# Kernel tuning notes

Measured on AMD Instinct MI355X. Metric: run time of the kernel, lower is better.

Reference implementation:

```python
import jax, jax.numpy as jnp
import numpy as np

SEQ_LEN = 2048
N_FFT = 4096   # rfft length n >= seq_len (repo uses next power of two of ~2*seq)
K = 24         # num_eigh
D = 768        # n_embd
BATCH = 1


def _spectral_filters(seq_len: int, k: int) -> jnp.ndarray:
    # Hankel matrix Z[i,j] = 2 / ((i+j)^3 - (i+j)), 1-indexed
    e = np.arange(1, seq_len + 1, dtype=np.float64)
    ipj = e[:, None] + e[None, :]
    Z = 2.0 / (ipj ** 3 - ipj)
    sigma, phi = np.linalg.eigh(Z)
    sigma, phi = sigma[-k:], phi[:, -k:]
    phi = phi * sigma ** 0.25
    return jnp.asarray(phi, dtype=jnp.float32)  # (seq_len, K)


def setup_inputs() -> dict:
    key = jax.random.key(0)
    k1, k2, k3 = jax.random.split(key, 3)
    x = jax.random.normal(k1, (BATCH, SEQ_LEN, D), dtype=jnp.float32)
    M_phi_plus = jax.random.normal(k2, (K, D, D), dtype=jnp.float32) * 0.02
    M_phi_minus = jax.random.normal(k3, (K, D, D), dtype=jnp.float32) * 0.02
    phi = _spectral_filters(SEQ_LEN, K)
    return {"x": x, "phi": phi, "M_phi_plus": M_phi_plus, "M_phi_minus": M_phi_minus}


def _convolve(u, v, n):
    # u: (b, seq, d), v: (seq, K)
    bsz, seq, d = u.shape
    k = v.shape[1]
    # alternating sign sequence (+1, -1, +1, ...)
    sgn = jnp.where(jnp.arange(seq) % 2 == 1, -1.0, 1.0)[None, :, None, None]  # (1,seq,1,1)
    V = jnp.fft.rfft(v.reshape(1, seq, k, 1, 1).astype(jnp.float32), n=n, axis=1)
    u4 = jnp.broadcast_to(u[:, :, None, :], (bsz, seq, k, d))  # (b,seq,K,d)
    U = jnp.stack([u4, u4 * sgn], axis=-1).astype(jnp.float32)  # (b,seq,K,d,2)
    Uf = jnp.fft.rfft(U, n=n, axis=1)
    U_conv = jnp.fft.irfft(V * Uf, n=n, axis=1)[:, :seq]  # (b,seq,K,d,2)
    U_plus = U_conv[..., 0]
    U_minus = U_conv[..., 1] * sgn
    return U_plus, U_minus


def reference(x, phi, M_phi_plus, M_phi_minus):
    U_plus, U_minus = _convolve(x, phi, N_FFT)
    spectral_plus = jnp.einsum('bskd,kde->bse', U_plus, M_phi_plus)
    spectral_minus = jnp.einsum('bskd,kde->bse', U_minus, M_phi_minus)
    return spectral_plus + spectral_minus
```

## Files before the change

### kernel.cpp

```cpp
#include <hip/hip_runtime.h>
#include <hip/hip_bf16.h>
#include <stdint.h>

#define SEQ 2048
#define DDIM 768
#define KF 24
#define NKV 48
#define NZC 8

typedef unsigned short ushort_t;
typedef __attribute__((ext_vector_type(8))) short short8;
typedef __attribute__((ext_vector_type(4))) float f32x4;

typedef __attribute__((address_space(3))) uint32_t lds_u32;
typedef __attribute__((address_space(1))) uint32_t glb_u32;

__device__ __forceinline__ unsigned short f2bf(float f) {
    union { float f; uint32_t u; } v; v.f = f;
    uint32_t u = v.u;
    return (unsigned short)((u + 0x7fff + ((u >> 16) & 1)) >> 16);
}


__global__ void k_pack_x(const float* __restrict__ x, ushort_t* __restrict__ xpk) {
    int b = blockIdx.x;
    int tt = b / 12, ks = b % 12;
    int tid = threadIdx.x;
    ushort_t* dst = xpk + (size_t)b * 8192;
    const float* src = x + (size_t)tt * 128 * DDIM + ks * 64;
#pragma unroll
    for (int p = 0; p < 4; ++p) {
        int s = p * 256 + tid;
        int row = s >> 3, sl = s & 7;
        const float* rp = src + (size_t)row * DDIM + sl * 8;
        float4 a = *(const float4*)rp;
        float4 c = *(const float4*)(rp + 4);
        ushort_t v[8] = {f2bf(a.x), f2bf(a.y), f2bf(a.z), f2bf(a.w),
                         f2bf(c.x), f2bf(c.y), f2bf(c.z), f2bf(c.w)};
        *(uint4*)(dst + row * 64 + ((sl ^ (row & 7)) << 3)) = *(uint4*)v;
    }
}

__global__ void k_pack_M(const float* __restrict__ Mp, const float* __restrict__ Mm,
                         ushort_t* __restrict__ Mpk) {
    __shared__ ushort_t lt[128 * 66];
    int b = blockIdx.x;
    int kv = b / 72; int rem = b % 72; int et = rem / 12, ks = rem % 12;
    const float* src = ((kv < KF) ? Mp + (size_t)kv * DDIM * DDIM
                                  : Mm + (size_t)(kv - KF) * DDIM * DDIM)
                       + (size_t)(ks * 64) * DDIM + et * 128;
    int tid = threadIdx.x;
#pragma unroll
    for (int p = 0; p < 32; ++p) {
        int lin = p * 256 + tid;
        int d = lin >> 7, e = lin & 127;
        lt[e * 66 + d] = f2bf(src[(size_t)d * DDIM + e]);
    }
    __syncthreads();
    ushort_t* dst = Mpk + (size_t)b * 8192;
#pragma unroll
    for (int p = 0; p < 4; ++p) {
        int s = p * 256 + tid; int row = s >> 3, sl = s & 7;
        ushort_t v[8];
#pragma unroll
        for (int j = 0; j < 8; ++j) v[j] = lt[row * 66 + sl * 8 + j];
        *(uint4*)(dst + row * 64 + ((sl ^ (row & 7)) << 3)) = *(uint4*)v;
    }
}

__global__ void k_build_T(const float* __restrict__ phi, ushort_t* __restrict__ Tpk) {
    __shared__ float phiL[256];
    int b = blockIdx.x;
    int kv = b / 17, slot = b % 17;
    int dm = slot - 1;
    int k = kv % KF; bool neg = kv >= KF;
    int tid = threadIdx.x;
    int tau = 128 * dm - 127 + tid;
    float v = 0.f;
    if (tid < 255 && tau >= 0 && tau < SEQ) {
        v = phi[(size_t)tau * KF + k];
        if (neg && (tau & 1)) v = -v;
    }
    phiL[tid] = v;
    __syncthreads();
    ushort_t* dst = Tpk + (size_t)b * 2 * 8192;
#pragma unroll
    for (int h = 0; h < 2; ++h) {
#pragma unroll
        for (int p = 0; p < 4; ++p) {
            int s = p * 256 + tid; int row = s >> 3, sl = s & 7;
            ushort_t v8[8];
#pragma unroll
            for (int j = 0; j < 8; ++j) {
                int col = h * 64 + sl * 8 + j;
                v8[j] = f2bf(phiL[row - col + 127]);
            }
            *(uint4*)(dst + h * 8192 + row * 64 + ((sl ^ (row & 7)) << 3)) = *(uint4*)v8;
        }
    }
}


__device__ __forceinline__ void read_frags(const ushort_t* As, const ushort_t* Bs,
                                           int lane, int wm, int wn, int kk,
                                           short8 av[4], short8 bv[4]) {
    int slot = kk * 4 + (lane >> 4);
#pragma unroll
    for (int m = 0; m < 4; ++m) {
        int row = wm * 64 + m * 16 + (lane & 15);
        av[m] = *(const short8*)(As + row * 64 + ((slot ^ (row & 7)) << 3));
    }
#pragma unroll
    for (int n = 0; n < 4; ++n) {
        int row = wn * 64 + n * 16 + (lane & 15);
        bv[n] = *(const short8*)(Bs + row * 64 + ((slot ^ (row & 7)) << 3));
    }
}

__device__ __forceinline__ void mfma16(const short8 av[4], const short8 bv[4], f32x4 acc[4][4]) {
    __builtin_amdgcn_s_setprio(1);
#pragma unroll
    for (int m = 0; m < 4; ++m)
#pragma unroll
        for (int n = 0; n < 4; ++n)
            acc[m][n] = __builtin_amdgcn_mfma_f32_16x16x32_bf16(av[m], bv[n], acc[m][n], 0, 0, 0);
    __builtin_amdgcn_s_setprio(0);
}

__global__ __launch_bounds__(256, 2)
void k_gemm_A(const ushort_t* __restrict__ Mpk, const ushort_t* __restrict__ xpk,
              ushort_t* __restrict__ Apk) {
    __shared__ ushort_t smem[2][2][8192];
    int bid = blockIdx.x;
    int kv = bid / 96; int rem = bid % 96; int et = rem / 16, tt = rem % 16;
    const ushort_t* Abase = Mpk + ((size_t)(kv * 6 + et) * 12) * 8192;
    const ushort_t* Bbase = xpk + (size_t)(tt * 12) * 8192;
    int tid = threadIdx.x, lane = tid & 63, wave = tid >> 6;
    int wm = wave >> 1, wn = wave & 1;

    auto stage4 = [&](const ushort_t* src, ushort_t* dst) {
        const char* s = (const char*)src + wave * 4096 + lane * 16;
        char* l = (char*)dst + wave * 4096;
#pragma unroll
        for (int p = 0; p < 4; ++p)
            __builtin_amdgcn_global_load_lds((const glb_u32*)(s + p * 1024),
                                             (lds_u32*)(l + p * 1024), 16, 0, 0);
    };

    f32x4 acc[4][4];
#pragma unroll
    for (int m = 0; m < 4; ++m)
#pragma unroll
        for (int n = 0; n < 4; ++n) acc[m][n] = (f32x4){0.f, 0.f, 0.f, 0.f};

    stage4(Abase, smem[0][0]);
    stage4(Bbase, smem[0][1]);

    for (int s = 0; s < 12; ++s) {
        int c = s & 1;
        bool more = (s + 1 < 12);
        if (more) {
            stage4(Abase + (s + 1) * 8192, smem[c ^ 1][0]);
            asm volatile("s_waitcnt vmcnt(4)" ::: "memory");
        } else {
            asm volatile("s_waitcnt vmcnt(0)" ::: "memory");
        }
        __builtin_amdgcn_s_barrier();
        __builtin_amdgcn_sched_barrier(0);

        const ushort_t* As = smem[c][0];
        const ushort_t* Bs = smem[c][1];
        short8 av0[4], bv0[4], av1[4], bv1[4];
        read_frags(As, Bs, lane, wm, wn, 0, av0, bv0);
        asm volatile("s_waitcnt lgkmcnt(0)" ::: "memory");
        __builtin_amdgcn_sched_barrier(0);
        read_frags(As, Bs, lane, wm, wn, 1, av1, bv1);
        if (more) stage4(Bbase + (s + 1) * 8192, smem[c ^ 1][1]);
        mfma16(av0, bv0, acc);
        asm volatile("s_waitcnt lgkmcnt(0)" ::: "memory");
        __builtin_amdgcn_sched_barrier(0);
        mfma16(av1, bv1, acc);
        __builtin_amdgcn_s_barrier();
    }

    ushort_t* sm = &smem[0][0][0];
#pragma unroll
    for (int m = 0; m < 4; ++m) {
        int rb = wm * 64 + m * 16 + ((lane >> 4) << 2);
#pragma unroll
        for (int n = 0; n < 4; ++n) {
            int cb = wn * 64 + n * 16 + (lane & 15);
            int h = cb >> 6, c6 = cb & 63, sl = c6 >> 3, j = c6 & 7;
#pragma unroll
            for (int r = 0; r < 4; ++r) {
                int row = rb + r;
                sm[h * 8192 + row * 64 + ((sl ^ (row & 7)) << 3) + j] = f2bf(acc[m][n][r]);
            }
        }
    }
    __syncthreads();
    uint4* d4 = (uint4*)(Apk + ((size_t)((kv * 6 + et) * 16 + tt) * 2) * 8192);
    const uint4* s4 = (const uint4*)sm;
#pragma unroll
    for (int p = 0; p < 8; ++p) d4[p * 256 + tid] = s4[p * 256 + tid];
}

__global__ __launch_bounds__(256, 2)
void k_gemm_Bv4(const ushort_t* __restrict__ Tpk, const ushort_t* __restrict__ Apk,
                float* __restrict__ outz) {
    __shared__ ushort_t smem[2][2][8192];

    int bid = blockIdx.x;
    int lid = (bid & 7) * 54 + (bid >> 3);
    int et = lid / 72;
    int cidx = lid % 72;
    int i1 = 0, zc = 0, base = 0;
#pragma unroll
    for (int t = 0; t < 16; ++t) {
        int cand = 15 - t;
        int nc = (cand >> 1) + 1;
        if (cidx < base + nc) { i1 = cand; zc = cidx - base; break; }
        base += nc;
    }
    int jlo = zc * 2;
    const int NS = NKV * 2 * 2;

    int tid = threadIdx.x, lane = tid & 63, wave = tid >> 6;
    int wm = wave >> 1, wn = wave & 1;

    f32x4 acc[4][4];
#pragma unroll
    for (int m = 0; m < 4; ++m)
#pragma unroll
        for (int n = 0; n < 4; ++n) acc[m][n] = (f32x4){0.f, 0.f, 0.f, 0.f};

    auto timg = [&](int kv, int jj, int h) -> const ushort_t* {
        return Tpk + ((size_t)((kv * 17 + (i1 - jj + 1)) * 2 + h)) * 8192;
    };
    auto aimg = [&](int kv, int jj, int h) -> const ushort_t* {
        return Apk + ((size_t)(((kv * 6 + et) * 16 + jj) * 2 + h)) * 8192;
    };
    auto stage4 = [&](const ushort_t* src, ushort_t* dst) {
        const char* s = (const char*)src + wave * 4096 + lane * 16;
        char* l = (char*)dst + wave * 4096;
#pragma unroll
        for (int p = 0; p < 4; ++p)
            __builtin_amdgcn_global_load_lds((const glb_u32*)(s + p * 1024),
                                             (lds_u32*)(l + p * 1024), 16, 0, 0);
    };

    int kv = 0, jj = jlo, h = 0;
    stage4(timg(kv, jj, h), smem[0][0]);
    stage4(aimg(kv, jj, h), smem[0][1]);

    for (int s = 0; s < NS; ++s) {
        int c = s & 1;
        int nh = h ^ 1, njj = jj, nkvv = kv;
        if (!nh) { njj = jj + 1; if (njj > jlo + 1) { njj = jlo; nkvv = kv + 1; } }
        bool more = (s + 1 < NS);

        if (more) {
            stage4(timg(nkvv, njj, nh), smem[c ^ 1][0]);
            asm volatile("s_waitcnt vmcnt(4)" ::: "memory");
        } else {
            asm volatile("s_waitcnt vmcnt(0)" ::: "memory");
        }
        __builtin_amdgcn_s_barrier();
        __builtin_amdgcn_sched_barrier(0);

        const ushort_t* As = smem[c][0];
        const ushort_t* Bs = smem[c][1];
        short8 av[2][4], bv[2][4];
#pragma unroll
        for (int kk = 0; kk < 2; ++kk) {
            int slot = kk * 4 + (lane >> 4);
#pragma unroll
            for (int m = 0; m < 4; ++m) {
                int row = wm * 64 + m * 16 + (lane & 15);
                av[kk][m] = *(const short8*)(As + row * 64 + ((slot ^ (row & 7)) << 3));
            }
#pragma unroll
            for (int n = 0; n < 4; ++n) {
                int row = wn * 64 + n * 16 + (lane & 15);
                bv[kk][n] = *(const short8*)(Bs + row * 64 + ((slot ^ (row & 7)) << 3));
            }
        }
        if (more) stage4(aimg(nkvv, njj, nh), smem[c ^ 1][1]);

        asm volatile("s_waitcnt lgkmcnt(0)" ::: "memory");
        __builtin_amdgcn_sched_barrier(0);

        __builtin_amdgcn_s_setprio(1);
#pragma unroll
        for (int kk = 0; kk < 2; ++kk)
#pragma unroll
            for (int m = 0; m < 4; ++m)
#pragma unroll
                for (int n = 0; n < 4; ++n)
                    acc[m][n] = __builtin_amdgcn_mfma_f32_16x16x32_bf16(av[kk][m], bv[kk][n], acc[m][n], 0, 0, 0);
        __builtin_amdgcn_s_setprio(0);
        __builtin_amdgcn_s_barrier();
        kv = nkvv; jj = njj; h = nh;
    }

    float* dst = outz + ((size_t)zc * SEQ + (size_t)i1 * 128) * DDIM + et * 128;
#pragma unroll
    for (int m = 0; m < 4; ++m) {
        int rb = wm * 64 + m * 16 + ((lane >> 4) << 2);
#pragma unroll
        for (int n = 0; n < 4; ++n) {
            int cb = wn * 64 + n * 16 + (lane & 15);
#pragma unroll
            for (int r = 0; r < 4; ++r)
                dst[(size_t)(rb + r) * DDIM + cb] = acc[m][n][r];
        }
    }
}

__global__ void k_reduce(const float* __restrict__ outz, float* __restrict__ out, int n4) {
    int idx = blockIdx.x * blockDim.x + threadIdx.x;
    if (idx < n4) {
        int srow = idx / (DDIM / 4);
        int zmax = srow >> 8;
        if (zmax > NZC - 1) zmax = NZC - 1;
        float4 s = ((const float4*)outz)[idx];
        for (int z = 1; z <= zmax; ++z) {
            float4 t = ((const float4*)(outz + (size_t)z * SEQ * DDIM))[idx];
            s.x += t.x; s.y += t.y; s.z += t.z; s.w += t.w;
        }
        ((float4*)out)[idx] = s;
    }
}

extern "C" void kernel_launch(void* const* d_in, const int* in_sizes, int n_in,
                              void* d_out, int out_size, void* d_ws, size_t ws_size,
                              hipStream_t stream) {
    (void)in_sizes; (void)n_in;
    const float* x   = (const float*)d_in[0];
    const float* phi = (const float*)d_in[1];
    const float* Mp  = (const float*)d_in[2];
    const float* Mm  = (const float*)d_in[3];
    float* out = (float*)d_out;

    char* ws = (char*)d_ws;
    size_t off = 0;
    auto alloc = [&](size_t bytes) { size_t o = off; off += (bytes + 255) & ~(size_t)255; return o; };
    size_t o_xpk = alloc((size_t)16 * 12 * 8192 * 2);
    size_t o_Mpk = alloc((size_t)NKV * 6 * 12 * 8192 * 2);
    size_t o_Tpk = alloc((size_t)NKV * 17 * 2 * 8192 * 2);
    size_t o_Apk = alloc((size_t)NKV * 6 * 16 * 2 * 8192 * 2);
    if (off > ws_size) {
        hipMemsetAsync(d_out, 0, (size_t)out_size * 4, stream);
        return;
    }

    ushort_t* xpk = (ushort_t*)(ws + o_xpk);
    ushort_t* Mpk = (ushort_t*)(ws + o_Mpk);
    ushort_t* Tpk = (ushort_t*)(ws + o_Tpk);
    ushort_t* Apk = (ushort_t*)(ws + o_Apk);
    float*   outz = (float*)(ws + o_Mpk);

    k_pack_x<<<16 * 12, 256, 0, stream>>>(x, xpk);
    k_pack_M<<<NKV * 6 * 12, 256, 0, stream>>>(Mp, Mm, Mpk);
    k_build_T<<<NKV * 17, 256, 0, stream>>>(phi, Tpk);
    k_gemm_A<<<NKV * 96, 256, 0, stream>>>(Mpk, xpk, Apk);
    k_gemm_Bv4<<<432, 256, 0, stream>>>(Tpk, Apk, outz);
    int n4 = SEQ * DDIM / 4;
    k_reduce<<<(n4 + 255) / 256, 256, 0, stream>>>(outz, out, n4);
}
```

Before: 328.2 us.

## Stream-K schedule for Toeplitz GEMM with per-tile partial slabs and reduce

Replaces the uneven triangular tile split (432 blocks, each doing a fixed 192 k-steps on chunk pairs) with a stream-K decomposition. The full linearized iteration space of 78336 steps is divided evenly over 512 blocks of 153 steps each. Each block flushes a partial 128x128 tile to a slab whenever its output tile changes, and the reduce kernel sums the partial slabs covering each tile. The goal is better load balance and fuller use of the CUs, at the cost of extra partial-tile stores and a different reduce pattern.

```diff
diff --git a/kernel.cpp b/kernel.cpp
--- a/kernel.cpp
+++ b/kernel.cpp
@@ -6,7 +6,6 @@
 #define DDIM 768
 #define KF 24
 #define NKV 48
-#define NZC 8
 
 typedef unsigned short ushort_t;
 typedef __attribute__((ext_vector_type(8))) short short8;
@@ -206,24 +205,33 @@
 }
 
 __global__ __launch_bounds__(256, 2)
-void k_gemm_Bv4(const ushort_t* __restrict__ Tpk, const ushort_t* __restrict__ Apk,
-                float* __restrict__ outz) {
+void k_gemm_Bsk(const ushort_t* __restrict__ Tpk, const ushort_t* __restrict__ Apk,
+                float* __restrict__ slab) {
     __shared__ ushort_t smem[2][2][8192];
 
     int bid = blockIdx.x;
-    int lid = (bid & 7) * 54 + (bid >> 3);
-    int et = lid / 72;
-    int cidx = lid % 72;
-    int i1 = 0, zc = 0, base = 0;
-#pragma unroll
-    for (int t = 0; t < 16; ++t) {
-        int cand = 15 - t;
-        int nc = (cand >> 1) + 1;
-        if (cidx < base + nc) { i1 = cand; zc = cidx - base; break; }
-        base += nc;
-    }
-    int jlo = zc * 2;
-    const int NS = NKV * 2 * 2;
+    int lid = (bid & 7) * 64 + (bid >> 3);
+    int g0 = lid * 153;
+
+    int ce = g0 / 13056;
+    int r  = g0 - ce * 13056;
+    int ci = 0;
+    while (48 * (ci + 1) * (ci + 2) <= r) ++ci;
+    int rr = r - 48 * ci * (ci + 1);
+    int cj = rr / 96;
+    int q  = rr - cj * 96;
+    int ck = q >> 1, ch = q & 1;
+
+    int ne = ce, ni = ci, nj = cj, nk = ck, nh = ch;
+    auto adv = [&]() {
+        nh ^= 1;
+        if (!nh) {
+            if (++nk == NKV) { nk = 0;
+                if (++nj > ni) { nj = 0;
+                    if (++ni == 16) { ni = 0; ++ne; } } }
+        }
+    };
+    adv();
 
     int tid = threadIdx.x, lane = tid & 63, wave = tid >> 6;
     int wm = wave >> 1, wn = wave & 1;
@@ -234,11 +242,11 @@
 #pragma unroll
         for (int n = 0; n < 4; ++n) acc[m][n] = (f32x4){0.f, 0.f, 0.f, 0.f};
 
-    auto timg = [&](int kv, int jj, int h) -> const ushort_t* {
-        return Tpk + ((size_t)((kv * 17 + (i1 - jj + 1)) * 2 + h)) * 8192;
-    };
-    auto aimg = [&](int kv, int jj, int h) -> const ushort_t* {
-        return Apk + ((size_t)(((kv * 6 + et) * 16 + jj) * 2 + h)) * 8192;
+    auto timgf = [&](int i1_, int jj_, int kv_, int h_) -> const ushort_t* {
+        return Tpk + ((size_t)((kv_ * 17 + (i1_ - jj_ + 1)) * 2 + h_)) * 8192;
+    };
+    auto aimgf = [&](int et_, int jj_, int kv_, int h_) -> const ushort_t* {
+        return Apk + ((size_t)(((kv_ * 6 + et_) * 16 + jj_) * 2 + h_)) * 8192;
     };
     auto stage4 = [&](const ushort_t* src, ushort_t* dst) {
         const char* s = (const char*)src + wave * 4096 + lane * 16;
@@ -249,18 +257,15 @@
                                              (lds_u32*)(l + p * 1024), 16, 0, 0);
     };
 
-    int kv = 0, jj = jlo, h = 0;
-    stage4(timg(kv, jj, h), smem[0][0]);
-    stage4(aimg(kv, jj, h), smem[0][1]);
-
-    for (int s = 0; s < NS; ++s) {
+    stage4(timgf(ci, cj, ck, ch), smem[0][0]);
+    stage4(aimgf(ce, cj, ck, ch), smem[0][1]);
+
+    for (int s = 0; s < 153; ++s) {
         int c = s & 1;
-        int nh = h ^ 1, njj = jj, nkvv = kv;
-        if (!nh) { njj = jj + 1; if (njj > jlo + 1) { njj = jlo; nkvv = kv + 1; } }
-        bool more = (s + 1 < NS);
+        bool more = (s + 1 < 153);
 
         if (more) {
-            stage4(timg(nkvv, njj, nh), smem[c ^ 1][0]);
+            stage4(timgf(ni, nj, nk, nh), smem[c ^ 1][0]);
             asm volatile("s_waitcnt vmcnt(4)" ::: "memory");
         } else {
             asm volatile("s_waitcnt vmcnt(0)" ::: "memory");
@@ -285,7 +290,7 @@
                 bv[kk][n] = *(const short8*)(Bs + row * 64 + ((slot ^ (row & 7)) << 3));
             }
         }
-        if (more) stage4(aimg(nkvv, njj, nh), smem[c ^ 1][1]);
+        if (more) stage4(aimgf(ne, nj, nk, nh), smem[c ^ 1][1]);
 
         asm volatile("s_waitcnt lgkmcnt(0)" ::: "memory");
         __builtin_amdgcn_sched_barrier(0);
@@ -300,33 +305,45 @@
                     acc[m][n] = __builtin_amdgcn_mfma_f32_16x16x32_bf16(av[kk][m], bv[kk][n], acc[m][n], 0, 0, 0);
         __builtin_amdgcn_s_setprio(0);
         __builtin_amdgcn_s_barrier();
-        kv = nkvv; jj = njj; h = nh;
-    }
-
-    float* dst = outz + ((size_t)zc * SEQ + (size_t)i1 * 128) * DDIM + et * 128;
-#pragma unroll
-    for (int m = 0; m < 4; ++m) {
-        int rb = wm * 64 + m * 16 + ((lane >> 4) << 2);
-#pragma unroll
-        for (int n = 0; n < 4; ++n) {
-            int cb = wn * 64 + n * 16 + (lane & 15);
-#pragma unroll
-            for (int r = 0; r < 4; ++r)
-                dst[(size_t)(rb + r) * DDIM + cb] = acc[m][n][r];
-        }
-    }
-}
-
-__global__ void k_reduce(const float* __restrict__ outz, float* __restrict__ out, int n4) {
+
+        if (!more || ni != ci || ne != ce) {
+            float* dst = slab + (size_t)(lid + ce * 16 + ci) * 16384;
+#pragma unroll
+            for (int m = 0; m < 4; ++m) {
+                int rb = wm * 64 + m * 16 + ((lane >> 4) << 2);
+#pragma unroll
+                for (int n = 0; n < 4; ++n) {
+                    int cb = wn * 64 + n * 16 + (lane & 15);
+#pragma unroll
+                    for (int rr2 = 0; rr2 < 4; ++rr2) {
+                        dst[(rb + rr2) * 128 + cb] = acc[m][n][rr2];
+                        acc[m][n][rr2] = 0.f;
+                    }
+                }
+            }
+        }
+        ce = ne; ci = ni; cj = nj; ck = nk; ch = nh;
+        adv();
+    }
+}
+
+__global__ void k_reduce(const float* __restrict__ slab, float* __restrict__ out, int n4) {
     int idx = blockIdx.x * blockDim.x + threadIdx.x;
     if (idx < n4) {
         int srow = idx / (DDIM / 4);
-        int zmax = srow >> 8;
-        if (zmax > NZC - 1) zmax = NZC - 1;
-        float4 s = ((const float4*)outz)[idx];
-        for (int z = 1; z <= zmax; ++z) {
-            float4 t = ((const float4*)(outz + (size_t)z * SEQ * DDIM))[idx];
-            s.x += t.x; s.y += t.y; s.z += t.z; s.w += t.w;
+        int e4 = idx % (DDIM / 4);
+        int i1 = srow >> 7;
+        int et = e4 >> 5;
+        int t = et * 16 + i1;
+        int T0 = et * 13056 + 48 * i1 * (i1 + 1);
+        int len = 96 * (i1 + 1);
+        int bs = T0 / 153;
+        int be = (T0 + len - 1) / 153;
+        size_t elem = (size_t)(srow & 127) * 128 + ((e4 * 4) & 127);
+        float4 s = {0.f, 0.f, 0.f, 0.f};
+        for (int b = bs; b <= be; ++b) {
+            float4 v = *(const float4*)(slab + (size_t)(b + t) * 16384 + elem);
+            s.x += v.x; s.y += v.y; s.z += v.z; s.w += v.w;
         }
         ((float4*)out)[idx] = s;
     }
@@ -358,13 +375,13 @@
     ushort_t* Mpk = (ushort_t*)(ws + o_Mpk);
     ushort_t* Tpk = (ushort_t*)(ws + o_Tpk);
     ushort_t* Apk = (ushort_t*)(ws + o_Apk);
-    float*   outz = (float*)(ws + o_Mpk);
+    float*   slab = (float*)(ws + o_Mpk);
 
     k_pack_x<<<16 * 12, 256, 0, stream>>>(x, xpk);
     k_pack_M<<<NKV * 6 * 12, 256, 0, stream>>>(Mp, Mm, Mpk);
     k_build_T<<<NKV * 17, 256, 0, stream>>>(phi, Tpk);
     k_gemm_A<<<NKV * 96, 256, 0, stream>>>(Mpk, xpk, Apk);
-    k_gemm_Bv4<<<432, 256, 0, stream>>>(Tpk, Apk, outz);
+    k_gemm_Bsk<<<512, 256, 0, stream>>>(Tpk, Apk, slab);
     int n4 = SEQ * DDIM / 4;
-    k_reduce<<<(n4 + 255) / 256, 256, 0, stream>>>(outz, out, n4);
-}
+    k_reduce<<<(n4 + 255) / 256, 256, 0, stream>>>(slab, out, n4);
+}
```

After: 503.3 us. +53.3%, slower.

## Rebalance Toeplitz GEMM work split across more blocks with mixed chunk sizes

Applied to the files above, without the earlier changes.

Reworks how the block-Toeplitz GEMM is divided among workgroups. Blocks now carry either two or one j-tiles, giving 600 blocks instead of 432 with split-K chunks of different sizes. The reduce kernel is updated to sum up to 8 partial slices per row group. The aim is better load balance and CU occupancy, at the cost of more partial outputs to write and reduce.

```diff
diff --git a/kernel.cpp b/kernel.cpp
--- a/kernel.cpp
+++ b/kernel.cpp
@@ -206,24 +206,40 @@
 }
 
 __global__ __launch_bounds__(256, 2)
-void k_gemm_Bv4(const ushort_t* __restrict__ Tpk, const ushort_t* __restrict__ Apk,
+void k_gemm_Bv5(const ushort_t* __restrict__ Tpk, const ushort_t* __restrict__ Apk,
                 float* __restrict__ outz) {
     __shared__ ushort_t smem[2][2][8192];
 
     int bid = blockIdx.x;
-    int lid = (bid & 7) * 54 + (bid >> 3);
-    int et = lid / 72;
-    int cidx = lid % 72;
-    int i1 = 0, zc = 0, base = 0;
-#pragma unroll
-    for (int t = 0; t < 16; ++t) {
-        int cand = 15 - t;
-        int nc = (cand >> 1) + 1;
-        if (cidx < base + nc) { i1 = cand; zc = cidx - base; break; }
-        base += nc;
-    }
-    int jlo = zc * 2;
-    const int NS = NKV * 2 * 2;
+    int et, i1, zc, nj;
+    if (bid < 216) {
+        int l = (bid & 7) * 27 + (bid >> 3);
+        et = l / 36; int r = l % 36;
+        int u = 0;
+#pragma unroll
+        for (int t = 1; t < 8; ++t) if (r >= t * (t + 1) / 2) u = t;
+        zc = r - u * (u + 1) / 2;
+        i1 = u + 8; nj = 2;
+    } else {
+        int b2 = bid - 216;
+        int l = (b2 & 7) * 48 + (b2 >> 3);
+        et = l / 64; int r = l % 64;
+        if (r < 36) {
+            int u = 0;
+#pragma unroll
+            for (int t = 1; t < 8; ++t) if (r >= t * (t + 1) / 2) u = t;
+            i1 = u; zc = r - u * (u + 1) / 2;
+        } else {
+            int r2 = r - 36;
+            int v = 0;
+#pragma unroll
+            for (int t = 1; t <= 6; ++t) { int pf = 7 * t - t * (t - 1) / 2; if (r2 >= pf) v = t; }
+            i1 = 8 + v;
+            zc = (v + 1) + (r2 - (7 * v - v * (v - 1) / 2));
+        }
+        nj = 1;
+    }
+    const int NS = 96 * nj;
 
     int tid = threadIdx.x, lane = tid & 63, wave = tid >> 6;
     int wm = wave >> 1, wn = wave & 1;
@@ -234,6 +250,11 @@
 #pragma unroll
         for (int n = 0; n < 4; ++n) acc[m][n] = (f32x4){0.f, 0.f, 0.f, 0.f};
 
+    auto coords = [&](int s, int& kv, int& jj, int& h) {
+        h = s & 1; int t = s >> 1;
+        if (nj == 2) { jj = (t & 1) ? zc + 8 : zc; kv = t >> 1; }
+        else { jj = zc; kv = t; }
+    };
     auto timg = [&](int kv, int jj, int h) -> const ushort_t* {
         return Tpk + ((size_t)((kv * 17 + (i1 - jj + 1)) * 2 + h)) * 8192;
     };
@@ -249,18 +270,19 @@
                                              (lds_u32*)(l + p * 1024), 16, 0, 0);
     };
 
-    int kv = 0, jj = jlo, h = 0;
+    int kv, jj, h;
+    coords(0, kv, jj, h);
     stage4(timg(kv, jj, h), smem[0][0]);
     stage4(aimg(kv, jj, h), smem[0][1]);
 
     for (int s = 0; s < NS; ++s) {
         int c = s & 1;
-        int nh = h ^ 1, njj = jj, nkvv = kv;
-        if (!nh) { njj = jj + 1; if (njj > jlo + 1) { njj = jlo; nkvv = kv + 1; } }
         bool more = (s + 1 < NS);
+        int nkv, njj, nh;
+        if (more) coords(s + 1, nkv, njj, nh); else { nkv = kv; njj = jj; nh = h; }
 
         if (more) {
-            stage4(timg(nkvv, njj, nh), smem[c ^ 1][0]);
+            stage4(timg(nkv, njj, nh), smem[c ^ 1][0]);
             asm volatile("s_waitcnt vmcnt(4)" ::: "memory");
         } else {
             asm volatile("s_waitcnt vmcnt(0)" ::: "memory");
@@ -285,7 +307,7 @@
                 bv[kk][n] = *(const short8*)(Bs + row * 64 + ((slot ^ (row & 7)) << 3));
             }
         }
-        if (more) stage4(aimg(nkvv, njj, nh), smem[c ^ 1][1]);
+        if (more) stage4(aimg(nkv, njj, nh), smem[c ^ 1][1]);
 
         asm volatile("s_waitcnt lgkmcnt(0)" ::: "memory");
         __builtin_amdgcn_sched_barrier(0);
@@ -300,7 +322,7 @@
                     acc[m][n] = __builtin_amdgcn_mfma_f32_16x16x32_bf16(av[kk][m], bv[kk][n], acc[m][n], 0, 0, 0);
         __builtin_amdgcn_s_setprio(0);
         __builtin_amdgcn_s_barrier();
-        kv = nkvv; jj = njj; h = nh;
+        kv = nkv; jj = njj; h = nh;
     }
 
     float* dst = outz + ((size_t)zc * SEQ + (size_t)i1 * 128) * DDIM + et * 128;
@@ -321,7 +343,7 @@
     int idx = blockIdx.x * blockDim.x + threadIdx.x;
     if (idx < n4) {
         int srow = idx / (DDIM / 4);
-        int zmax = srow >> 8;
+        int zmax = srow >> 7;
         if (zmax > NZC - 1) zmax = NZC - 1;
         float4 s = ((const float4*)outz)[idx];
         for (int z = 1; z <= zmax; ++z) {
@@ -364,7 +386,7 @@
     k_pack_M<<<NKV * 6 * 12, 256, 0, stream>>>(Mp, Mm, Mpk);
     k_build_T<<<NKV * 17, 256, 0, stream>>>(phi, Tpk);
     k_gemm_A<<<NKV * 96, 256, 0, stream>>>(Mpk, xpk, Apk);
-    k_gemm_Bv4<<<432, 256, 0, stream>>>(Tpk, Apk, outz);
+    k_gemm_Bv5<<<600, 256, 0, stream>>>(Tpk, Apk, outz);
     int n4 = SEQ * DDIM / 4;
     k_reduce<<<(n4 + 255) / 256, 256, 0, stream>>>(outz, out, n4);
 }
```

Result: no change. 332.3 us (+1.3%).
